# Performance work log

Measured on AMD Instinct MI355X. Metric: run time of the kernel, lower is better.

The kernel has to match this reference:

```python
import jax, jax.numpy as jnp
import numpy as np

LMAX, MMAX = 4, 2
C = 128          # sphere_channels
MOUT = 128       # m_output_channels
N = 32768        # number of edges
K = sum(2 * min(l, MMAX) + 1 for l in range(LMAX + 1))  # 19 coefficients
LN_EPS = 1e-5


def build_to_m():
    # l-major ordering of (l, m) coefficients -> m-major permutation matrix
    ms = np.array([m for l in range(LMAX + 1)
                   for m in range(-min(l, MMAX), min(l, MMAX) + 1)])
    order = list(np.nonzero(ms == 0)[0])
    for m in range(1, MMAX + 1):
        order += list(np.nonzero(ms == m)[0]) + list(np.nonzero(ms == -m)[0])
    P = np.zeros((K, K), np.float32)
    P[np.arange(K), order] = 1.0
    return jnp.asarray(P)


TO_M = build_to_m()
M_SIZE = [LMAX + 1] + [LMAX - m + 1 for m in range(1, MMAX + 1)]  # [5, 4, 3]


def _layernorm(h, g, b):
    mu = jnp.mean(h, axis=-1, keepdims=True)
    var = jnp.mean(jnp.square(h - mu), axis=-1, keepdims=True)
    return (h - mu) * jax.lax.rsqrt(var + LN_EPS) * g + b


def _radial_mlp(x, w1, b1, g1, be1, w2, b2, g2, be2, w3, b3):
    h = jax.nn.silu(_layernorm(x @ w1.T + b1, g1, be1))
    h = jax.nn.silu(_layernorm(h @ w2.T + b2, g2, be2))
    return h @ w3.T + b3  # [N, 1536]


def setup_inputs() -> dict:
    key = jax.random.key(0)
    ks = jax.random.split(key, 16)
    s = 0.02
    return {
        "x": jax.random.normal(ks[0], (N, K, C), jnp.float32),
        "x_edge": jax.random.normal(ks[1], (N, C), jnp.float32),
        "fc0_w": jax.random.normal(ks[2], (MOUT * 5, 5 * C), jnp.float32) * s,
        "fc0_b": jax.random.normal(ks[3], (MOUT * 5,), jnp.float32) * s,
        "fc1_w": jax.random.normal(ks[4], (MOUT * 4, 4 * C), jnp.float32) * s,
        "fc2_w": jax.random.normal(ks[5], (MOUT * 3, 3 * C), jnp.float32) * s,
        "rad_w1": jax.random.normal(ks[6], (C, C), jnp.float32) * s,
        "rad_b1": jax.random.normal(ks[7], (C,), jnp.float32) * s,
        "rad_g1": jnp.ones((C,), jnp.float32),
        "rad_beta1": jnp.zeros((C,), jnp.float32),
        "rad_w2": jax.random.normal(ks[8], (C, C), jnp.float32) * s,
        "rad_b2": jax.random.normal(ks[9], (C,), jnp.float32) * s,
        "rad_g2": jnp.ones((C,), jnp.float32),
        "rad_beta2": jnp.zeros((C,), jnp.float32),
        "rad_w3": jax.random.normal(ks[10], (1536, C), jnp.float32) * s,
        "rad_b3": jax.random.normal(ks[11], (1536,), jnp.float32) * s,
    }


def reference(x, x_edge, fc0_w, fc0_b, fc1_w, fc2_w,
              rad_w1, rad_b1, rad_g1, rad_beta1,
              rad_w2, rad_b2, rad_g2, rad_beta2,
              rad_w3, rad_b3):
    n = x.shape[0]
    # reorder coefficients by m (to_m is a permutation)
    xm = jnp.einsum('nac,ba->nbc', x, TO_M)
    rad = _radial_mlp(x_edge, rad_w1, rad_b1, rad_g1, rad_beta1,
                      rad_w2, rad_b2, rad_g2, rad_beta2, rad_w3, rad_b3)

    # m = 0 block
    sz0 = M_SIZE[0]
    x0 = xm[:, :sz0].reshape(n, sz0 * C) * rad[:, :sz0 * C]
    y0 = (x0 @ fc0_w.T + fc0_b).reshape(n, sz0, MOUT)
    outs = [y0]

    offset, offr = sz0, sz0 * C
    for m, fcw in zip((1, 2), (fc1_w, fc2_w)):
        sz = M_SIZE[m]
        din = sz * C
        xb = xm[:, offset:offset + 2 * sz].reshape(n, 2, din)
        xb = xb * rad[:, offr:offr + din][:, None, :]  # FiLM radial scale
        yb = (xb @ fcw.T).reshape(n, 2 * sz, MOUT)
        outs.append(yb)
        offset += 2 * sz
        offr += din

    out = jnp.concatenate(outs, axis=1)  # [N, K, MOUT]
    # project back from m-major ordering
    return jnp.einsum('nac,ab->nbc', out, TO_M)
```

## Files before the change

### kernel.cpp

```cpp
#include <hip/hip_runtime.h>

typedef __bf16 bf16x8 __attribute__((ext_vector_type(8)));
typedef __bf16 bf16x4 __attribute__((ext_vector_type(4)));
typedef float f32x4 __attribute__((ext_vector_type(4)));

#define MFMA_16x16x32_BF16(a, b, c) __builtin_amdgcn_mfma_f32_16x16x32_bf16(a, b, c, 0, 0, 0)

typedef const __attribute__((address_space(1))) unsigned int* gas_ptr;
typedef __attribute__((address_space(3))) unsigned int* las_ptr;

__device__ __forceinline__ void gload_lds16(const void* g, void* l) {
    __builtin_amdgcn_global_load_lds((gas_ptr)(unsigned long long)g,
                                     (las_ptr)(unsigned long long)l, 16, 0, 0);
}

__constant__ int ORDER_C[19] = {0, 2, 6, 11, 16, 3, 7, 12, 17, 1, 5, 10, 15, 8, 13, 18, 4, 9, 14};

__global__ __launch_bounds__(256) void wxconv_kernel(
    const float* __restrict__ fc0, const float* __restrict__ fc1,
    const float* __restrict__ fc2, const float* __restrict__ rw1,
    const float* __restrict__ rw2, const float* __restrict__ rw3,
    const float* __restrict__ xe, __bf16* __restrict__ wo,
    __bf16* __restrict__ xo) {
    const int bid = blockIdx.x;
    const float* s;
    __bf16* o;
    int i4, rel;
    if (bid < 1024) {
        i4 = (bid * 256 + threadIdx.x) * 4;
        o = wo;
        if (i4 < 409600)      { s = fc0; rel = i4; }
        else if (i4 < 671744) { s = fc1; rel = i4 - 409600; }
        else if (i4 < 819200) { s = fc2; rel = i4 - 671744; }
        else if (i4 < 835584) { s = rw1; rel = i4 - 819200; }
        else if (i4 < 851968) { s = rw2; rel = i4 - 835584; }
        else                  { s = rw3; rel = i4 - 851968; }
    } else {
        i4 = ((bid - 1024) * 256 + threadIdx.x) * 4;
        o = xo; s = xe; rel = i4;
    }
    float4 v = *(const float4*)(s + rel);
    bf16x4 b;
    b[0] = (__bf16)v.x; b[1] = (__bf16)v.y; b[2] = (__bf16)v.z; b[3] = (__bf16)v.w;
    *(bf16x4*)(o + i4) = b;
}

__global__ __launch_bounds__(256) void gemmln_kernel(
    const __bf16* __restrict__ Ain, const __bf16* __restrict__ Wb,
    const float* __restrict__ bvec, const float* __restrict__ gv,
    const float* __restrict__ bev, __bf16* __restrict__ hs) {
    __shared__ __align__(16) char smem[65536];
    __bf16* As = (__bf16*)smem;
    __bf16* Bs = (__bf16*)(smem + 32768);
    float*  Fs = (float*)smem;
    const int tid = threadIdx.x;
    const int w = tid >> 6, lane = tid & 63;
    const int quad = lane >> 4, l16 = lane & 15;
    const int e0 = blockIdx.x * 128;

    {
        const char* ga = (const char*)(Ain + (size_t)e0 * 128);
        const char* gb = (const char*)Wb;
        for (int r = 0; r < 8; ++r) {
            int boff = (r * 4 + w) * 1024 + lane * 16;
            int soff = boff ^ (((boff >> 8) & 15) << 4);
            gload_lds16(ga + soff, (char*)As + boff);
            gload_lds16(gb + soff, (char*)Bs + boff);
        }
    }
    __syncthreads();

    const int wr = w >> 1, wc = w & 1;
    f32x4 acc[4][4] = {};
    for (int ks = 0; ks < 4; ++ks) {
        bf16x8 af[4], bfr[4];
        for (int i = 0; i < 4; ++i) {
            int ar = wr * 64 + i * 16 + l16;
            af[i] = *(const bf16x8*)&As[ar * 128 + ((ks * 32 + quad * 8) ^ ((ar & 15) << 3))];
        }
        for (int j = 0; j < 4; ++j) {
            int br = wc * 64 + j * 16 + l16;
            bfr[j] = *(const bf16x8*)&Bs[br * 128 + ((ks * 32 + quad * 8) ^ ((br & 15) << 3))];
        }
        for (int i = 0; i < 4; ++i)
            for (int j = 0; j < 4; ++j)
                acc[i][j] = MFMA_16x16x32_BF16(af[i], bfr[j], acc[i][j]);
    }
    __syncthreads();

    float bc[4];
    for (int j = 0; j < 4; ++j) bc[j] = bvec[wc * 64 + j * 16 + l16];
    for (int i = 0; i < 4; ++i)
        for (int j = 0; j < 4; ++j)
            for (int r = 0; r < 4; ++r)
                Fs[(wr * 64 + i * 16 + quad * 4 + r) * 128 + wc * 64 + j * 16 + l16] =
                    acc[i][j][r] + bc[j];
    __syncthreads();

    const float gl = gv[lane], gh = gv[lane + 64];
    const float bl = bev[lane], bh = bev[lane + 64];
    for (int it = 0; it < 32; ++it) {
        const int row = it * 4 + w;
        float a = Fs[row * 128 + lane];
        float b = Fs[row * 128 + lane + 64];
        float s = a + b;
        s += __shfl_xor(s, 1);  s += __shfl_xor(s, 2);  s += __shfl_xor(s, 4);
        s += __shfl_xor(s, 8);  s += __shfl_xor(s, 16); s += __shfl_xor(s, 32);
        const float mu = s * (1.f / 128.f);
        const float da = a - mu, db = b - mu;
        float v = da * da + db * db;
        v += __shfl_xor(v, 1);  v += __shfl_xor(v, 2);  v += __shfl_xor(v, 4);
        v += __shfl_xor(v, 8);  v += __shfl_xor(v, 16); v += __shfl_xor(v, 32);
        const float rs = rsqrtf(v * (1.f / 128.f) + 1e-5f);
        float ya = da * rs * gl + bl;
        float yb = db * rs * gh + bh;
        ya = ya / (1.f + __expf(-ya));
        yb = yb / (1.f + __expf(-yb));
        hs[(size_t)(e0 + row) * 128 + lane] = (__bf16)ya;
        hs[(size_t)(e0 + row) * 128 + lane + 64] = (__bf16)yb;
    }
}

__global__ __launch_bounds__(256) void radial3_kernel(
    const __bf16* __restrict__ h2g, const __bf16* __restrict__ w3b,
    const float* __restrict__ b3, __bf16* __restrict__ radg) {
    __shared__ __align__(16) __bf16 As[128 * 128];
    __shared__ __align__(16) __bf16 Bs[128 * 128];
    const int tid = threadIdx.x;
    const int w = tid >> 6, lane = tid & 63;
    const int quad = lane >> 4, l16 = lane & 15;
    const int e0 = blockIdx.x * 128, n0 = blockIdx.y * 128;

    {
        const char* ga = (const char*)(h2g + (size_t)e0 * 128);
        const char* gb = (const char*)(w3b + (size_t)n0 * 128);
        for (int r = 0; r < 8; ++r) {
            int boff = (r * 4 + w) * 1024 + lane * 16;
            int soff = boff ^ (((boff >> 8) & 15) << 4);
            gload_lds16(ga + soff, (char*)As + boff);
            gload_lds16(gb + soff, (char*)Bs + boff);
        }
    }
    __syncthreads();

    const int wr = w >> 1, wc = w & 1;
    f32x4 acc[4][4] = {};
    for (int ks = 0; ks < 4; ++ks) {
        bf16x8 af[4], bfr[4];
        for (int i = 0; i < 4; ++i) {
            int ar = wr * 64 + i * 16 + l16;
            af[i] = *(const bf16x8*)&As[ar * 128 + ((ks * 32 + quad * 8) ^ ((ar & 15) << 3))];
        }
        for (int j = 0; j < 4; ++j) {
            int br = wc * 64 + j * 16 + l16;
            bfr[j] = *(const bf16x8*)&Bs[br * 128 + ((ks * 32 + quad * 8) ^ ((br & 15) << 3))];
        }
        for (int i = 0; i < 4; ++i)
            for (int j = 0; j < 4; ++j)
                acc[i][j] = MFMA_16x16x32_BF16(af[i], bfr[j], acc[i][j]);
    }
    __syncthreads();

    float bcol[4];
    for (int j = 0; j < 4; ++j) bcol[j] = b3[n0 + wc * 64 + j * 16 + l16];
    for (int i = 0; i < 4; ++i)
        for (int j = 0; j < 4; ++j)
            for (int r = 0; r < 4; ++r) {
                int row = wr * 64 + i * 16 + quad * 4 + r;
                int col = wc * 64 + j * 16 + l16;
                As[row * 128 + col] = (__bf16)(acc[i][j][r] + bcol[j]);
            }
    __syncthreads();
    for (int r = 0; r < 8; ++r) {
        int idx = r * 256 + tid;
        int e = idx >> 4, c = (idx & 15) * 8;
        *(uint4*)(radg + (size_t)(e0 + e) * 1536 + n0 + c) = *(const uint4*)&As[e * 128 + c];
    }
}

__global__ __launch_bounds__(256) void so2_main_kernel(
    const float* __restrict__ xg, const __bf16* __restrict__ radg,
    const __bf16* __restrict__ wfc0, const __bf16* __restrict__ wfc1,
    const __bf16* __restrict__ wfc2, const float* __restrict__ fc0b,
    float* __restrict__ outg) {
    __shared__ __align__(16) __bf16 As[128 * 64];
    __shared__ __align__(16) __bf16 Bs[128 * 64];
    const int tid = threadIdx.x;
    const int w = tid >> 6, lane = tid & 63;
    const int quad = lane >> 4, l16 = lane & 15;
    const int e0 = blockIdx.x * 128;
    const int gid = blockIdx.y;

    const int bstart = (gid == 0) ? 0 : (gid == 1) ? 5 : (gid == 2) ? 9 : (gid == 3) ? 13 : 16;
    const int sz     = (gid == 0) ? 5 : (gid < 3) ? 4 : 3;
    const int rado   = (gid == 0) ? 0 : (gid < 3) ? 640 : 1152;
    const int K      = sz * 128;
    const __bf16* W  = (gid == 0) ? wfc0 : (gid < 3) ? wfc1 : wfc2;

    const int wr = w >> 1, wc = w & 1;
    const int e_ = tid >> 4;
    const int cA = (tid & 15) * 4;

    for (int so = 0; so < sz; ++so) {
        f32x4 acc[4][4] = {};
        const char* wbase = (const char*)W + ((size_t)so * 128 * K) * 2;
        const int nkt = 2 * sz;
        for (int kt = 0; kt < nkt; ++kt) {
            const int s_in = kt >> 1, cb = (kt & 1) * 64;
            const int xrow = ORDER_C[bstart + s_in];
            {
                const float* xp = xg + (size_t)(e0 + e_) * 2432 + xrow * 128 + cb + cA;
                const __bf16* rp = radg + (size_t)(e0 + e_) * 1536 + rado + s_in * 128 + cb + cA;
                for (int r = 0; r < 8; ++r) {
                    float4 xv = *(const float4*)(xp + (size_t)r * 16 * 2432);
                    bf16x4 rv = *(const bf16x4*)(rp + (size_t)r * 16 * 1536);
                    bf16x4 av;
                    av[0] = (__bf16)(xv.x * (float)rv[0]);
                    av[1] = (__bf16)(xv.y * (float)rv[1]);
                    av[2] = (__bf16)(xv.z * (float)rv[2]);
                    av[3] = (__bf16)(xv.w * (float)rv[3]);
                    const int arow = e_ + r * 16;
                    *(bf16x4*)&As[arow * 64 + (cA ^ ((arow & 7) << 3))] = av;
                }
            }
            {
                const char* wkt = wbase + (size_t)kt * 128;
                for (int r = 0; r < 4; ++r) {
                    int boff = (r * 4 + w) * 1024 + lane * 16;
                    int col = boff >> 7, kb = boff & 127;
                    gload_lds16(wkt + (size_t)col * K * 2 + (kb ^ ((col & 7) << 4)),
                                (char*)Bs + boff);
                }
            }
            __syncthreads();
            for (int ks = 0; ks < 2; ++ks) {
                bf16x8 af[4], bfr[4];
                for (int i = 0; i < 4; ++i) {
                    int ar = wr * 64 + i * 16 + l16;
                    af[i] = *(const bf16x8*)&As[ar * 64 + ((ks * 32 + quad * 8) ^ ((ar & 7) << 3))];
                }
                for (int j = 0; j < 4; ++j) {
                    int br = wc * 64 + j * 16 + l16;
                    bfr[j] = *(const bf16x8*)&Bs[br * 64 + ((ks * 32 + quad * 8) ^ ((br & 7) << 3))];
                }
                for (int i = 0; i < 4; ++i)
                    for (int j = 0; j < 4; ++j)
                        acc[i][j] = MFMA_16x16x32_BF16(af[i], bfr[j], acc[i][j]);
            }
            __syncthreads();
        }

        const int outrow = ORDER_C[bstart + so];
        float bv[4];
        for (int j = 0; j < 4; ++j)
            bv[j] = (gid == 0) ? fc0b[so * 128 + wc * 64 + j * 16 + l16] : 0.f;
        for (int i = 0; i < 4; ++i)
            for (int j = 0; j < 4; ++j) {
                const int col = wc * 64 + j * 16 + l16;
                for (int r = 0; r < 4; ++r) {
                    const int row = e0 + wr * 64 + i * 16 + quad * 4 + r;
                    outg[(size_t)row * 2432 + outrow * 128 + col] = acc[i][j][r] + bv[j];
                }
            }
    }
}

extern "C" void kernel_launch(void* const* d_in, const int* in_sizes, int n_in,
                              void* d_out, int out_size, void* d_ws, size_t ws_size,
                              hipStream_t stream) {
    const float* x       = (const float*)d_in[0];
    const float* x_edge  = (const float*)d_in[1];
    const float* fc0_w   = (const float*)d_in[2];
    const float* fc0_b   = (const float*)d_in[3];
    const float* fc1_w   = (const float*)d_in[4];
    const float* fc2_w   = (const float*)d_in[5];
    const float* rad_w1  = (const float*)d_in[6];
    const float* rad_b1  = (const float*)d_in[7];
    const float* rad_g1  = (const float*)d_in[8];
    const float* rad_be1 = (const float*)d_in[9];
    const float* rad_w2  = (const float*)d_in[10];
    const float* rad_b2  = (const float*)d_in[11];
    const float* rad_g2  = (const float*)d_in[12];
    const float* rad_be2 = (const float*)d_in[13];
    const float* rad_w3  = (const float*)d_in[14];
    const float* rad_b3  = (const float*)d_in[15];
    float* out = (float*)d_out;

    const int N = in_sizes[0] / (19 * 128);

    __bf16* wb  = (__bf16*)d_ws;
    __bf16* sh  = (__bf16*)((char*)d_ws + (2u << 20));
    __bf16* rb  = (__bf16*)((char*)d_ws + (10u << 20));
    __bf16* h1  = rb;
    __bf16* rad = rb;
    __bf16* wfc0 = wb;
    __bf16* wfc1 = wb + 409600;
    __bf16* wfc2 = wb + 671744;
    __bf16* w1b  = wb + 819200;
    __bf16* w2b  = wb + 835584;
    __bf16* w3b  = wb + 851968;

    wxconv_kernel<<<dim3(5120), dim3(256), 0, stream>>>(fc0_w, fc1_w, fc2_w, rad_w1,
                                                        rad_w2, rad_w3, x_edge, wb, sh);
    gemmln_kernel<<<dim3(N / 128), dim3(256), 0, stream>>>(sh, w1b, rad_b1, rad_g1,
                                                           rad_be1, h1);
    gemmln_kernel<<<dim3(N / 128), dim3(256), 0, stream>>>(h1, w2b, rad_b2, rad_g2,
                                                           rad_be2, sh);
    radial3_kernel<<<dim3(N / 128, 12), dim3(256), 0, stream>>>(sh, w3b, rad_b3, rad);
    so2_main_kernel<<<dim3(N / 128, 5), dim3(256), 0, stream>>>(x, rad, wfc0, wfc1, wfc2,
                                                                fc0_b, out);
}
```

Measured before the change: 857.1 us.

## Fuse FiLM scaling into radial GEMM epilogue and double-buffer SO2 GEMM

The radial third-layer kernel now multiplies its output tile by the matching x rows in its epilogue and writes the FiLM-scaled bf16 A operand, laid out in m-major order, to workspace. The SO2 GEMM no longer does per-tile float conversion of x times rad. It loads A and W straight into LDS with double-buffered async loads, and each block computes one output coefficient over a grid of 19 instead of 5. This removes the redundant re-reads and conversion of x and rad across output slices, at the cost of a larger bf16 intermediate buffer in workspace and a third of the work per SO2 block.

```diff
diff --git a/kernel.cpp b/kernel.cpp
--- a/kernel.cpp
+++ b/kernel.cpp
@@ -121,15 +121,17 @@
     }
 }
 
-__global__ __launch_bounds__(256) void radial3_kernel(
+__global__ __launch_bounds__(256) void radial3_film_kernel(
     const __bf16* __restrict__ h2g, const __bf16* __restrict__ w3b,
-    const float* __restrict__ b3, __bf16* __restrict__ radg) {
+    const float* __restrict__ b3, const float* __restrict__ xg,
+    __bf16* __restrict__ Aws) {
     __shared__ __align__(16) __bf16 As[128 * 128];
     __shared__ __align__(16) __bf16 Bs[128 * 128];
     const int tid = threadIdx.x;
     const int w = tid >> 6, lane = tid & 63;
     const int quad = lane >> 4, l16 = lane & 15;
-    const int e0 = blockIdx.x * 128, n0 = blockIdx.y * 128;
+    const int y = blockIdx.y;
+    const int e0 = blockIdx.x * 128, n0 = y * 128;
 
     {
         const char* ga = (const char*)(h2g + (size_t)e0 * 128);
@@ -171,98 +173,109 @@
                 As[row * 128 + col] = (__bf16)(acc[i][j][r] + bcol[j]);
             }
     __syncthreads();
-    for (int r = 0; r < 8; ++r) {
-        int idx = r * 256 + tid;
-        int e = idx >> 4, c = (idx & 15) * 8;
-        *(uint4*)(radg + (size_t)(e0 + e) * 1536 + n0 + c) = *(const uint4*)&As[e * 128 + c];
-    }
-}
-
-__global__ __launch_bounds__(256) void so2_main_kernel(
-    const float* __restrict__ xg, const __bf16* __restrict__ radg,
-    const __bf16* __restrict__ wfc0, const __bf16* __restrict__ wfc1,
-    const __bf16* __restrict__ wfc2, const float* __restrict__ fc0b,
-    float* __restrict__ outg) {
-    __shared__ __align__(16) __bf16 As[128 * 64];
-    __shared__ __align__(16) __bf16 Bs[128 * 64];
+
+    int nb, bs0, bs1;
+    if (y < 5)      { nb = 1; bs0 = y;     bs1 = 0; }
+    else if (y < 9) { nb = 2; bs0 = y;     bs1 = y + 4; }
+    else            { nb = 2; bs0 = y + 4; bs1 = y + 7; }
+
+    for (int t = 0; t < nb; ++t) {
+        const int b = t ? bs1 : bs0;
+        const int xrow = ORDER_C[b];
+        for (int r = 0; r < 8; ++r) {
+            int idx = r * 256 + tid;
+            int e = idx >> 4, c = (idx & 15) * 8;
+            bf16x8 rv = *(const bf16x8*)&As[e * 128 + c];
+            const float* xp = xg + (size_t)(e0 + e) * 2432 + xrow * 128 + c;
+            float4 x0 = *(const float4*)xp;
+            float4 x1 = *(const float4*)(xp + 4);
+            bf16x8 av;
+            av[0] = (__bf16)(x0.x * (float)rv[0]);
+            av[1] = (__bf16)(x0.y * (float)rv[1]);
+            av[2] = (__bf16)(x0.z * (float)rv[2]);
+            av[3] = (__bf16)(x0.w * (float)rv[3]);
+            av[4] = (__bf16)(x1.x * (float)rv[4]);
+            av[5] = (__bf16)(x1.y * (float)rv[5]);
+            av[6] = (__bf16)(x1.z * (float)rv[6]);
+            av[7] = (__bf16)(x1.w * (float)rv[7]);
+            *(bf16x8*)(Aws + (size_t)(e0 + e) * 2432 + b * 128 + c) = av;
+        }
+    }
+}
+
+__global__ __launch_bounds__(256) void so2_gemm_kernel(
+    const __bf16* __restrict__ Aws, const __bf16* __restrict__ wfc0,
+    const __bf16* __restrict__ wfc1, const __bf16* __restrict__ wfc2,
+    const float* __restrict__ fc0b, float* __restrict__ outg) {
+    __shared__ __align__(16) __bf16 As[2][128 * 64];
+    __shared__ __align__(16) __bf16 Bs[2][128 * 64];
     const int tid = threadIdx.x;
     const int w = tid >> 6, lane = tid & 63;
     const int quad = lane >> 4, l16 = lane & 15;
     const int e0 = blockIdx.x * 128;
-    const int gid = blockIdx.y;
-
-    const int bstart = (gid == 0) ? 0 : (gid == 1) ? 5 : (gid == 2) ? 9 : (gid == 3) ? 13 : 16;
-    const int sz     = (gid == 0) ? 5 : (gid < 3) ? 4 : 3;
-    const int rado   = (gid == 0) ? 0 : (gid < 3) ? 640 : 1152;
-    const int K      = sz * 128;
-    const __bf16* W  = (gid == 0) ? wfc0 : (gid < 3) ? wfc1 : wfc2;
+    const int y = blockIdx.y;
+
+    int bstart, sz;
+    const __bf16* W;
+    if (y < 5)       { bstart = 0;  sz = 5; W = wfc0; }
+    else if (y < 9)  { bstart = 5;  sz = 4; W = wfc1; }
+    else if (y < 13) { bstart = 9;  sz = 4; W = wfc1; }
+    else if (y < 16) { bstart = 13; sz = 3; W = wfc2; }
+    else             { bstart = 16; sz = 3; W = wfc2; }
+    const int K = sz * 128, s_out = y - bstart, nkt = 2 * sz;
+    const char* abase = (const char*)Aws + (size_t)bstart * 256;
+    const char* wbase = (const char*)W + (size_t)s_out * 128 * K * 2;
+
+#define STAGE(buf, kt)                                                             \
+    {                                                                              \
+        const char* ak = abase + (size_t)(kt) * 128;                               \
+        const char* wk = wbase + (size_t)(kt) * 128;                               \
+        for (int r = 0; r < 4; ++r) {                                              \
+            int boff = (r * 4 + w) * 1024 + lane * 16;                             \
+            int row = boff >> 7, kb = boff & 127;                                  \
+            int skb = kb ^ ((row & 7) << 4);                                       \
+            gload_lds16(ak + (size_t)(e0 + row) * 4864 + skb, (char*)As[buf] + boff); \
+            gload_lds16(wk + (size_t)row * (size_t)(K * 2) + skb, (char*)Bs[buf] + boff); \
+        }                                                                          \
+    }
 
     const int wr = w >> 1, wc = w & 1;
-    const int e_ = tid >> 4;
-    const int cA = (tid & 15) * 4;
-
-    for (int so = 0; so < sz; ++so) {
-        f32x4 acc[4][4] = {};
-        const char* wbase = (const char*)W + ((size_t)so * 128 * K) * 2;
-        const int nkt = 2 * sz;
-        for (int kt = 0; kt < nkt; ++kt) {
-            const int s_in = kt >> 1, cb = (kt & 1) * 64;
-            const int xrow = ORDER_C[bstart + s_in];
-            {
-                const float* xp = xg + (size_t)(e0 + e_) * 2432 + xrow * 128 + cb + cA;
-                const __bf16* rp = radg + (size_t)(e0 + e_) * 1536 + rado + s_in * 128 + cb + cA;
-                for (int r = 0; r < 8; ++r) {
-                    float4 xv = *(const float4*)(xp + (size_t)r * 16 * 2432);
-                    bf16x4 rv = *(const bf16x4*)(rp + (size_t)r * 16 * 1536);
-                    bf16x4 av;
-                    av[0] = (__bf16)(xv.x * (float)rv[0]);
-                    av[1] = (__bf16)(xv.y * (float)rv[1]);
-                    av[2] = (__bf16)(xv.z * (float)rv[2]);
-                    av[3] = (__bf16)(xv.w * (float)rv[3]);
-                    const int arow = e_ + r * 16;
-                    *(bf16x4*)&As[arow * 64 + (cA ^ ((arow & 7) << 3))] = av;
-                }
+    f32x4 acc[4][4] = {};
+    STAGE(0, 0);
+    __syncthreads();
+    for (int kt = 0; kt < nkt; ++kt) {
+        const int cur = kt & 1;
+        if (kt + 1 < nkt) STAGE(cur ^ 1, kt + 1);
+        for (int ks = 0; ks < 2; ++ks) {
+            bf16x8 af[4], bfr[4];
+            for (int i = 0; i < 4; ++i) {
+                int ar = wr * 64 + i * 16 + l16;
+                af[i] = *(const bf16x8*)&As[cur][ar * 64 + ((ks * 32 + quad * 8) ^ ((ar & 7) << 3))];
             }
-            {
-                const char* wkt = wbase + (size_t)kt * 128;
-                for (int r = 0; r < 4; ++r) {
-                    int boff = (r * 4 + w) * 1024 + lane * 16;
-                    int col = boff >> 7, kb = boff & 127;
-                    gload_lds16(wkt + (size_t)col * K * 2 + (kb ^ ((col & 7) << 4)),
-                                (char*)Bs + boff);
-                }
+            for (int j = 0; j < 4; ++j) {
+                int br = wc * 64 + j * 16 + l16;
+                bfr[j] = *(const bf16x8*)&Bs[cur][br * 64 + ((ks * 32 + quad * 8) ^ ((br & 7) << 3))];
             }
-            __syncthreads();
-            for (int ks = 0; ks < 2; ++ks) {
-                bf16x8 af[4], bfr[4];
-                for (int i = 0; i < 4; ++i) {
-                    int ar = wr * 64 + i * 16 + l16;
-                    af[i] = *(const bf16x8*)&As[ar * 64 + ((ks * 32 + quad * 8) ^ ((ar & 7) << 3))];
-                }
-                for (int j = 0; j < 4; ++j) {
-                    int br = wc * 64 + j * 16 + l16;
-                    bfr[j] = *(const bf16x8*)&Bs[br * 64 + ((ks * 32 + quad * 8) ^ ((br & 7) << 3))];
-                }
-                for (int i = 0; i < 4; ++i)
-                    for (int j = 0; j < 4; ++j)
-                        acc[i][j] = MFMA_16x16x32_BF16(af[i], bfr[j], acc[i][j]);
+            for (int i = 0; i < 4; ++i)
+                for (int j = 0; j < 4; ++j)
+                    acc[i][j] = MFMA_16x16x32_BF16(af[i], bfr[j], acc[i][j]);
+        }
+        __syncthreads();
+    }
+#undef STAGE
+
+    const int outrow = ORDER_C[y];
+    float bv[4];
+    for (int j = 0; j < 4; ++j)
+        bv[j] = (y < 5) ? fc0b[s_out * 128 + wc * 64 + j * 16 + l16] : 0.f;
+    for (int i = 0; i < 4; ++i)
+        for (int j = 0; j < 4; ++j) {
+            const int col = wc * 64 + j * 16 + l16;
+            for (int r = 0; r < 4; ++r) {
+                const int row = e0 + wr * 64 + i * 16 + quad * 4 + r;
+                outg[(size_t)row * 2432 + outrow * 128 + col] = acc[i][j][r] + bv[j];
             }
-            __syncthreads();
-        }
-
-        const int outrow = ORDER_C[bstart + so];
-        float bv[4];
-        for (int j = 0; j < 4; ++j)
-            bv[j] = (gid == 0) ? fc0b[so * 128 + wc * 64 + j * 16 + l16] : 0.f;
-        for (int i = 0; i < 4; ++i)
-            for (int j = 0; j < 4; ++j) {
-                const int col = wc * 64 + j * 16 + l16;
-                for (int r = 0; r < 4; ++r) {
-                    const int row = e0 + wr * 64 + i * 16 + quad * 4 + r;
-                    outg[(size_t)row * 2432 + outrow * 128 + col] = acc[i][j][r] + bv[j];
-                }
-            }
-    }
+        }
 }
 
 extern "C" void kernel_launch(void* const* d_in, const int* in_sizes, int n_in,
@@ -290,9 +303,8 @@
 
     __bf16* wb  = (__bf16*)d_ws;
     __bf16* sh  = (__bf16*)((char*)d_ws + (2u << 20));
-    __bf16* rb  = (__bf16*)((char*)d_ws + (10u << 20));
-    __bf16* h1  = rb;
-    __bf16* rad = rb;
+    __bf16* Aws = (__bf16*)((char*)d_ws + (10u << 20));
+    __bf16* h1  = Aws;
     __bf16* wfc0 = wb;
     __bf16* wfc1 = wb + 409600;
     __bf16* wfc2 = wb + 671744;
@@ -306,7 +318,8 @@
                                                            rad_be1, h1);
     gemmln_kernel<<<dim3(N / 128), dim3(256), 0, stream>>>(h1, w2b, rad_b2, rad_g2,
                                                            rad_be2, sh);
-    radial3_kernel<<<dim3(N / 128, 12), dim3(256), 0, stream>>>(sh, w3b, rad_b3, rad);
-    so2_main_kernel<<<dim3(N / 128, 5), dim3(256), 0, stream>>>(x, rad, wfc0, wfc1, wfc2,
-                                                                fc0_b, out);
-}
+    radial3_film_kernel<<<dim3(N / 128, 12), dim3(256), 0, stream>>>(sh, w3b, rad_b3,
+                                                                     x, Aws);
+    so2_gemm_kernel<<<dim3(N / 128, 19), dim3(256), 0, stream>>>(Aws, wfc0, wfc1, wfc2,
+                                                                 fc0_b, out);
+}
```

After: 760.7 us. 11.2% less time.
